# Performance work log

Measured on AMD Instinct MI355X. Metric: run time of the kernel, lower is better.

The kernel has to match this reference:

```python
import jax, jax.numpy as jnp
import numpy as np

N_MSB = 4      # bit planes
WB = 8         # weight quant bits
ABNM = 8       # activation quant bits (non-MVM)
NL = 0.1       # noise level


def quant(x, bits, r):
    # quant_pass: symmetric round-to-grid inside [-r, r]
    s = 2.0 ** (bits - 1)
    xs = jnp.clip(x / r, -1.0 + 1.0 / s, 1.0 - 1.0 / s)
    return jnp.round(xs * s) / s * r


def pact(x, a):
    # pact_a reduces to a hard clip to [-a, a]
    return jnp.clip(x, -a, a)


def bitsplit(x, n_msb):
    # x in [0,1] -> n_msb binary planes y[i] and beta weights l2/l1
    l1 = 2.0 ** n_msb - 1.0
    l2 = 2.0 ** (n_msb - 1 - jnp.arange(n_msb, dtype=x.dtype))  # [n_msb]
    y = jnp.floor(jnp.round(l1 * x)[None] / l2[:, None, None]) % 2.0  # [n_msb,B,D]
    return y, l2 / l1


def noisy_bmm(inp, W, b, key):
    # CustomMM_bmm.forward: quantized weights + additive gaussian noise
    kw, kb = jax.random.split(key)
    nw = jax.lax.stop_gradient(jax.random.normal(kw, W.shape, W.dtype) * W.max() * NL)
    nb = jax.lax.stop_gradient(jax.random.normal(kb, b.shape, b.dtype) * b.max() * NL)
    wq = quant(W, WB, 1.0)
    bq = quant(b, WB, 1.0)
    return jnp.einsum('mbi,mio->mbo', inp, wq + nw) + bq + nb  # [n_msb,B,4H]


def setup_inputs() -> dict:
    key = jax.random.key(0)
    ks = jax.random.split(key, 9)
    B, I, H, M = 4096, 256, 1024, N_MSB
    inp = {
        'input': jax.random.normal(ks[0], (B, I), jnp.float32),
        'hx': jax.random.normal(ks[1], (B, H), jnp.float32),
        'cx': jax.random.normal(ks[2], (B, H), jnp.float32),
        'weight_ih': jax.random.normal(ks[3], (M, I, 4 * H), jnp.float32),
        'weight_hh': jax.random.normal(ks[4], (M, H, 4 * H), jnp.float32),
        'bias_ih': jax.random.normal(ks[5], (M, 1, 4 * H), jnp.float32),
        'bias_hh': jax.random.normal(ks[6], (M, 1, 4 * H), jnp.float32),
        'a1': jnp.array([128.0], jnp.float32),
        'a3': jnp.array([1.0], jnp.float32),
        'a4': jnp.array([1.0], jnp.float32),
        'a5': jnp.array([1.0], jnp.float32),
        'a6': jnp.array([1.0], jnp.float32),
        'a7': jnp.array([4.0], jnp.float32),
        'a8': jnp.array([1.0], jnp.float32),
        'a9': jnp.array([4.0], jnp.float32),
        'a10': jnp.array([1.0], jnp.float32),
        'a11': jnp.array([4.0], jnp.float32),
    }
    return inp


def reference(input, hx, cx, weight_ih, weight_hh, bias_ih, bias_hh,
              a1, a3, a4, a5, a6, a7, a8, a9, a10, a11):
    k1, k2 = jax.random.split(jax.random.key(42))
    # input branch: clip -> map to [0,1] -> bit-split -> noisy bmm -> threshold -> beta-sum
    inp01 = (pact(input, a1) + a1) / (a1 * 2)
    y, beta = bitsplit(inp01, N_MSB)
    out = (noisy_bmm(y, weight_ih, bias_ih, k1) > 0.5).astype(input.dtype)
    part1 = (beta[:, None, None] * out).sum(0) * (a1 * 2) - a1
    # hidden branch (note: '+ a1' offset as in the original source)
    inp01 = (pact(hx, a11) + a1) / (a11 * 2)
    y, beta = bitsplit(inp01, N_MSB)
    out = (noisy_bmm(y, weight_hh, bias_hh, k2) > 0.5).astype(input.dtype)
    part2 = (beta[:, None, None] * out).sum(0) * (a11 * 2) - a11
    gates = part1 + part2  # [B, 4H]
    i, j, f, o = jnp.split(gates, 4, axis=1)
    fg = quant(pact(jax.nn.sigmoid(f), a3), ABNM, a3)
    ig = quant(pact(jax.nn.sigmoid(i), a4), ABNM, a4)
    act = quant(pact(jnp.tanh(j), a5), ABNM, a5)
    og = quant(pact(jax.nn.sigmoid(o), a6), ABNM, a6)
    gated_cell = quant(pact(cx * fg, a7), ABNM, a7)
    activated_input = quant(pact(ig * act, a8), ABNM, a8)
    new_c = quant(pact(gated_cell + activated_input, a9), ABNM, a9)
    activated_cell = quant(pact(jnp.tanh(new_c), a10), ABNM, a10)
    new_h = quant(pact(activated_cell * og, a11), ABNM, a11)
    return new_h, new_c
```

## Files before the change

### kernel.cpp

```cpp
#include <hip/hip_runtime.h>
#include <cstdint>
#include <cstddef>


typedef int v4i __attribute__((ext_vector_type(4)));

struct KPc { uint32_t a, b; };

__host__ __device__ constexpr KPc ctf(uint32_t k0, uint32_t k1v, uint32_t c0, uint32_t c1) {
  uint32_t ks2 = k0 ^ k1v ^ 0x1BD11BDAu;
  uint32_t x0 = c0 + k0;
  uint32_t x1 = c1 + k1v;
  uint32_t r0[4] = {13u, 15u, 26u, 6u};
  uint32_t r1[4] = {17u, 29u, 16u, 24u};
  uint32_t ks[3] = {k0, k1v, ks2};
  for (int g = 0; g < 5; ++g) {
    for (int j = 0; j < 4; ++j) {
      uint32_t rr = (g & 1) ? r1[j] : r0[j];
      x0 += x1;
      x1 = (x1 << rr) | (x1 >> (32u - rr));
      x1 ^= x0;
    }
    x0 += ks[(g + 1) % 3];
    x1 += ks[(g + 2) % 3] + (uint32_t)(g + 1);
  }
  return KPc{x0, x1};
}

constexpr KPc K1K  = ctf(0u, 42u, 0u, 0u);
constexpr KPc K2K  = ctf(0u, 42u, 0u, 1u);
constexpr KPc KWIH = ctf(K1K.a, K1K.b, 0u, 0u);
constexpr KPc KBIH = ctf(K1K.a, K1K.b, 0u, 1u);
constexpr KPc KWHH = ctf(K2K.a, K2K.b, 0u, 0u);
constexpr KPc KBHH = ctf(K2K.a, K2K.b, 0u, 1u);

__device__ __forceinline__ uint32_t tf_bits(uint32_t k0, uint32_t k1v, uint32_t j) {
  KPc r = ctf(k0, k1v, 0u, j);
  return r.a ^ r.b;
}

__device__ __forceinline__ unsigned encf(float f) {
  unsigned u = __float_as_uint(f);
  return (u & 0x80000000u) ? ~u : (u | 0x80000000u);
}
__device__ __forceinline__ float decf(unsigned e) {
  unsigned u = (e & 0x80000000u) ? (e & 0x7FFFFFFFu) : ~e;
  return __uint_as_float(u);
}

__device__ __forceinline__ void rmax_seg(const float* __restrict__ x, int n,
                                         unsigned* __restrict__ out, int rbid, int nblk) {
  unsigned best = 0u;
  for (int i = rbid * 256 + threadIdx.x; i < n; i += nblk * 256) {
    unsigned e = encf(x[i]);
    best = best > e ? best : e;
  }
  for (int off = 32; off > 0; off >>= 1) {
    unsigned o = __shfl_down(best, off, 64);
    best = best > o ? best : o;
  }
  __shared__ unsigned sm[4];
  int lane = threadIdx.x & 63, wv = threadIdx.x >> 6;
  if (lane == 0) sm[wv] = best;
  __syncthreads();
  if (threadIdx.x == 0) {
    unsigned b = sm[0];
    for (int i = 1; i < 4; ++i) b = b > sm[i] ? b : sm[i];
    atomicMax(out, b);
  }
}

__global__ void rmax_all_kernel(const float* __restrict__ wih, const float* __restrict__ whh,
                                const float* __restrict__ bih, const float* __restrict__ bhh,
                                unsigned* __restrict__ enc) {
  int b = blockIdx.x;
  if (b < 512)       rmax_seg(wih, 4 * 256 * 4096,  enc + 0, b,        512);
  else if (b < 1024) rmax_seg(whh, 4 * 1024 * 4096, enc + 1, b - 512,  512);
  else if (b < 1088) rmax_seg(bih, 16384,           enc + 2, b - 1024, 64);
  else               rmax_seg(bhh, 16384,           enc + 3, b - 1088, 64);
}

__device__ __forceinline__ float xla_log1p(float t) {
  float small = __fmul_rn(__fadd_rn(__fmul_rn(-0.5f, t), 1.0f), t);
  float large = logf(__fadd_rn(t, 1.0f));
  return (fabsf(t) < 1e-4f) ? small : large;
}

__device__ __forceinline__ float xla_erfinv(float x) {
  float w = -xla_log1p(-__fmul_rn(x, x));
  float p;
  if (w < 5.0f) {
    float ww = __fadd_rn(w, -2.5f);
    p = 2.81022636e-08f;
    p = __fadd_rn(3.43273939e-07f, __fmul_rn(p, ww));
    p = __fadd_rn(-3.5233877e-06f, __fmul_rn(p, ww));
    p = __fadd_rn(-4.39150654e-06f, __fmul_rn(p, ww));
    p = __fadd_rn(0.00021858087f, __fmul_rn(p, ww));
    p = __fadd_rn(-0.00125372503f, __fmul_rn(p, ww));
    p = __fadd_rn(-0.00417768164f, __fmul_rn(p, ww));
    p = __fadd_rn(0.246640727f, __fmul_rn(p, ww));
    p = __fadd_rn(1.50140941f, __fmul_rn(p, ww));
  } else {
    float ww = __fadd_rn(sqrtf(w), -3.0f);
    p = -0.000200214257f;
    p = __fadd_rn(0.000100950558f, __fmul_rn(p, ww));
    p = __fadd_rn(0.00134934322f, __fmul_rn(p, ww));
    p = __fadd_rn(-0.00367342844f, __fmul_rn(p, ww));
    p = __fadd_rn(0.00573950773f, __fmul_rn(p, ww));
    p = __fadd_rn(-0.0076224613f, __fmul_rn(p, ww));
    p = __fadd_rn(0.00943887047f, __fmul_rn(p, ww));
    p = __fadd_rn(1.00167406f, __fmul_rn(p, ww));
    p = __fadd_rn(2.83297682f, __fmul_rn(p, ww));
  }
  return __fmul_rn(p, x);
}

__device__ __forceinline__ float normal_from_bits(uint32_t bits) {
  float u01 = __uint_as_float((bits >> 9) | 0x3f800000u) - 1.0f;
  const float lo = -0x1.fffffep-1f;
  float u = fmaxf(lo, __fadd_rn(__fmul_rn(u01, 2.0f), lo));
  return __fmul_rn(0x1.6a09e6p+0f, xla_erfinv(u));
}

__device__ __forceinline__ float quantw(float x) {
  float xs = fminf(fmaxf(x, -0.9921875f), 0.9921875f);
  return __fmul_rn(rintf(__fmul_rn(xs, 128.0f)), 0.0078125f);
}

__device__ void do_kv(const float* __restrict__ x, const float* __restrict__ ap,
                      const float* __restrict__ offp, unsigned char* __restrict__ kvT,
                      int Kdim, int bx, int by, unsigned char* sh) {
  unsigned char (*tile)[65] = (unsigned char (*)[65])sh;
  const int tid = threadIdx.x;
  const int bt = bx * 64, it = by * 64;
  const float a = ap[0], off = offp[0];
#pragma unroll
  for (int e = 0; e < 16; ++e) {
    int idx = e * 256 + tid;
    int bl = idx >> 6, il = idx & 63;
    float v = fmaxf(-a, fminf(x[(size_t)(bt + bl) * Kdim + it + il], a));
    float t = __fdiv_rn(__fadd_rn(v, off), __fmul_rn(a, 2.0f));
    int k = (int)rintf(__fmul_rn(15.0f, t));
    tile[il][bl] = (unsigned char)(k & 15);
  }
  __syncthreads();
#pragma unroll
  for (int e = 0; e < 16; ++e) {
    int idx = e * 256 + tid;
    int il = idx >> 6, bl = idx & 63;
    kvT[(size_t)(it + il) * 4096 + bt + bl] = tile[il][bl];
  }
}

__device__ void do_aih(const float* __restrict__ input, const float* __restrict__ a1p,
                       signed char* __restrict__ A, int rbid) {
  int j = rbid * 256 + threadIdx.x;
  if (j >= 4096 * 256) return;
  float a = a1p[0];
  float v = fmaxf(-a, fminf(input[j], a));
  float t = __fdiv_rn(__fadd_rn(v, a), __fmul_rn(a, 2.0f));
  int kq = (int)rintf(__fmul_rn(15.0f, t));
  A[j]                  = (signed char)((kq >> 2) & 1);
  A[1048576 + j]        = (signed char)((kq >> 1) & 1);
  A[2097152 + j]        = (signed char)(kq & 1);
}

__device__ void do_ahh(const float* __restrict__ hx, const float* __restrict__ a11p,
                       const float* __restrict__ a1p, signed char* __restrict__ A, int rbid) {
  int j = rbid * 256 + threadIdx.x;
  if (j >= 4096 * 1024) return;
  float a = a11p[0], off = a1p[0];
  float v = fmaxf(-a, fminf(hx[j], a));
  float t = __fdiv_rn(__fadd_rn(v, off), __fmul_rn(a, 2.0f));
  int kq = (int)rintf(__fmul_rn(15.0f, t));
  A[j]                      = (signed char)((kq >> 3) & 1);
  A[(size_t)(1 << 22) + j]  = (signed char)((kq >> 2) & 1);
  A[(size_t)(2 << 22) + j]  = (signed char)((kq >> 1) & 1);
  A[(size_t)(3 << 22) + j]  = (signed char)(kq & 1);
}

__device__ void do_bias(const float* __restrict__ bsrc, float* __restrict__ bq,
                        float* __restrict__ nb, int n, const unsigned* __restrict__ encp,
                        uint32_t k0, uint32_t k1v, int rbid) {
  int j = rbid * 256 + threadIdx.x;
  if (j >= n) return;
  float bmax = decf(*encp);
  float nrm = normal_from_bits(tf_bits(k0, k1v, (uint32_t)j));
  bq[j] = quantw(bsrc[j]);
  nb[j] = __fmul_rn(__fmul_rn(nrm, bmax), 0.1f);
}

__device__ void do_t0(const float* __restrict__ W, float* __restrict__ T0,
                      const unsigned* __restrict__ encp, int rbid) {
  int j = rbid * 256 + threadIdx.x;
  if (j >= 1048576) return;
  float wmax = decf(*encp);
  float nrm = normal_from_bits(tf_bits(KWIH.a, KWIH.b, (uint32_t)j));
  float nw = __fmul_rn(__fmul_rn(nrm, wmax), 0.1f);
  T0[j] = __fadd_rn(quantw(W[j]), nw);
}

__device__ void do_bt(const float* __restrict__ W, signed char* __restrict__ Bt,
                      const unsigned* __restrict__ encp, int K, int m0, int nPlanes,
                      uint32_t k0k, uint32_t k1k, int bx, int by, int bz,
                      unsigned char* sh) {
  signed char* lhi = (signed char*)sh;
  signed char* llo = (signed char*)sh + 4352;
  const int tid = threadIdx.x;
  const int m = m0 + bz;
  const int kt = by * 64, ct = bx * 64;
  const float wmax = decf(*encp);
#pragma unroll 4
  for (int i = 0; i < 16; ++i) {
    int e = i * 256 + tid;
    int kl = e >> 6, cl = e & 63;
    uint32_t j = (uint32_t)(((m * K + kt + kl) << 12) + ct + cl);
    float nrm = normal_from_bits(tf_bits(k0k, k1k, j));
    float t = __fadd_rn(quantw(W[j]), __fmul_rn(__fmul_rn(nrm, wmax), 0.1f));
    int ti = (int)rintf(__fmul_rn(t, 6144.0f));
    int hi = (ti + 128) >> 8;
    int lo = ti - (hi << 8);
    lhi[cl * 68 + kl] = (signed char)hi;
    llo[cl * 68 + kl] = (signed char)lo;
  }
  __syncthreads();
  const size_t planeElems = (size_t)K << 12;
  signed char* bh = Bt + (size_t)bz * planeElems;
  signed char* bl = Bt + (size_t)(nPlanes + bz) * planeElems;
#pragma unroll 4
  for (int i = 0; i < 16; ++i) {
    int f = i * 256 + tid;
    int cl = f >> 6, kl = f & 63;
    size_t o = (size_t)(ct + cl) * K + kt + kl;
    bh[o] = lhi[cl * 68 + kl];
    bl[o] = llo[cl * 68 + kl];
  }
}

__global__ __launch_bounds__(256) void prep_all_kernel(
    const float* __restrict__ input, const float* __restrict__ hx,
    const float* __restrict__ wih, const float* __restrict__ whh,
    const float* __restrict__ bih, const float* __restrict__ bhh,
    const float* __restrict__ a1p, const float* __restrict__ a11p,
    const unsigned* __restrict__ enc,
    unsigned char* __restrict__ kvT, signed char* __restrict__ A_ih,
    signed char* __restrict__ A_hh, float* __restrict__ bq_ih, float* __restrict__ nb_ih,
    float* __restrict__ bq_hh, float* __restrict__ nb_hh, float* __restrict__ T0,
    signed char* __restrict__ Bt_hh, signed char* __restrict__ Bt_ih) {
  __shared__ __align__(16) unsigned char sh[8704];
  int b = blockIdx.x;
  if (b < 256) {
    do_kv(input, a1p, a1p, kvT, 256, b & 63, b >> 6, sh);
  } else if (b < 4352) {
    do_aih(input, a1p, A_ih, b - 256);
  } else if (b < 20736) {
    do_ahh(hx, a11p, a1p, A_hh, b - 4352);
  } else if (b < 20800) {
    do_bias(bih, bq_ih, nb_ih, 16384, enc + 2, KBIH.a, KBIH.b, b - 20736);
  } else if (b < 20864) {
    do_bias(bhh, bq_hh, nb_hh, 16384, enc + 3, KBHH.a, KBHH.b, b - 20800);
  } else if (b < 24960) {
    do_t0(wih, T0, enc + 0, b - 20864);
  } else if (b < 29056) {
    int t = b - 24960;
    do_bt(whh, Bt_hh, enc + 1, 1024, 0, 4, KWHH.a, KWHH.b, t & 63, (t >> 6) & 15, t >> 10, sh);
  } else {
    int t = b - 29056;
    do_bt(wih, Bt_ih, enc + 0, 256, 1, 3, KWIH.a, KWIH.b, t & 63, (t >> 6) & 3, t >> 8, sh);
  }
}

__global__ __launch_bounds__(256) void gemm_p0_kernel(
    const float* __restrict__ T0, const float* __restrict__ bq, const float* __restrict__ nb,
    const unsigned char* __restrict__ kvT, unsigned char* __restrict__ Kp) {
  const int tid = threadIdx.x, lane = tid & 63, wv = tid >> 6;
  const int c0 = blockIdx.x * 32;
  const int row = blockIdx.y * 256 + wv * 64 + lane;

  float acc[32];
#pragma unroll
  for (int j = 0; j < 32; ++j) acc[j] = 0.0f;

  const unsigned char* kvp = kvT + row;
#pragma unroll 2
  for (int k = 0; k < 256; ++k) {
    unsigned nib = kvp[(size_t)k << 12];
    float f = (float)((nib >> 3) & 1u);
    const float4* tp = (const float4*)(T0 + ((size_t)k << 12) + c0);
    float4 tv[8];
#pragma unroll
    for (int q = 0; q < 8; ++q) tv[q] = tp[q];
#pragma unroll
    for (int q = 0; q < 8; ++q) {
      acc[q * 4 + 0] = __builtin_fmaf(f, tv[q].x, acc[q * 4 + 0]);
      acc[q * 4 + 1] = __builtin_fmaf(f, tv[q].y, acc[q * 4 + 1]);
      acc[q * 4 + 2] = __builtin_fmaf(f, tv[q].z, acc[q * 4 + 2]);
      acc[q * 4 + 3] = __builtin_fmaf(f, tv[q].w, acc[q * 4 + 3]);
    }
  }

#pragma unroll
  for (int j = 0; j < 32; ++j) {
    int col = c0 + j;
    float s = __fadd_rn(__fadd_rn(acc[j], bq[col]), nb[col]);
    Kp[((size_t)row << 12) + col] = (s > 0.5f) ? (unsigned char)8 : (unsigned char)0;
  }
}

typedef __attribute__((address_space(3))) signed char lds_i8;
typedef __attribute__((address_space(1))) const signed char g_i8;

__device__ __forceinline__ void glds16(const signed char* g, signed char* l) {
  __builtin_amdgcn_global_load_lds((g_i8*)g, (lds_i8*)l, 16, 0, 0);
}

__global__ __launch_bounds__(256, 3) void gemm_mfma_kernel(
    const signed char* __restrict__ Ahh, const signed char* __restrict__ Bthh,
    const signed char* __restrict__ Aih, const signed char* __restrict__ Btih,
    const float* __restrict__ bqh, const float* __restrict__ nbh,
    const float* __restrict__ bqi, const float* __restrict__ nbi,
    unsigned char* __restrict__ Kp) {
  const int tid = threadIdx.x;
  const int lane = tid & 63, wv = tid >> 6;
  const int col0 = blockIdx.x * 64;
  const int row0 = blockIdx.y * 128;
  const int wrow = (wv >> 1) * 64;
  const int wcol = (wv & 1) * 32;

  __shared__ __align__(16) signed char smbuf[3][16384];
  const int HOFF = 8192, LOFF = 12288;

  const int l15 = lane & 15;
  const int cc  = (((lane >> 4) ^ ((lane >> 1) & 3)) << 4);
  const int xq  = ((((lane & 3) ^ ((lane >> 3) & 3))) << 4);
  const int lr  = lane >> 2;

  uint32_t k12[4][2];
#pragma unroll
  for (int rf = 0; rf < 4; ++rf) { k12[rf][0] = 0u; k12[rf][1] = 0u; }

  for (int sub = 0; sub < 7; ++sub) {
    int K, w;
    const signed char *A, *Bh, *Bl;
    const float *bqp, *nbp;
    if (sub < 4) {
      int m = sub;
      K = 1024;
      A  = Ahh  + ((size_t)m << 22);
      Bh = Bthh + ((size_t)m << 22);
      Bl = Bthh + ((size_t)(4 + m) << 22);
      bqp = bqh + (m << 12); nbp = nbh + (m << 12);
      w = (1 << (3 - m)) << 4;
    } else {
      int m = sub - 3;
      K = 256;
      A  = Aih  + ((size_t)(m - 1) << 20);
      Bh = Btih + ((size_t)(m - 1) << 20);
      Bl = Btih + ((size_t)(3 + m - 1) << 20);
      bqp = bqi + (m << 12); nbp = nbi + (m << 12);
      w = 1 << (3 - m);
    }

    const size_t soff = (size_t)lr * K + xq;
    const signed char* gA  = A  + (size_t)(row0 + 32 * wv) * K + soff;
    const signed char* gA2 = gA + (size_t)16 * K;
    const signed char* gH  = Bh + (size_t)(col0 + 16 * wv) * K + soff;
    const signed char* gL  = Bl + (size_t)(col0 + 16 * wv) * K + soff;

    auto stage = [&](signed char* base, int k0) {
      glds16(gA  + k0, base + (32 * wv) * 64);
      glds16(gA2 + k0, base + (32 * wv + 16) * 64);
      glds16(gH  + k0, base + HOFF + (16 * wv) * 64);
      glds16(gL  + k0, base + LOFF + (16 * wv) * 64);
    };

    v4i ach[4][2], acl[4][2];
    v4i zero = {0, 0, 0, 0};
#pragma unroll
    for (int rf = 0; rf < 4; ++rf)
#pragma unroll
      for (int cf = 0; cf < 2; ++cf) { ach[rf][cf] = zero; acl[rf][cf] = zero; }

    signed char* bc = &smbuf[0][0];
    signed char* bn = &smbuf[1][0];
    signed char* bf = &smbuf[2][0];

    const int nt = K >> 6;
    stage(bc, 0);
    stage(bn, 64);

    for (int t = 0; t < nt; ++t) {
      if (t + 1 < nt) {
        asm volatile("s_waitcnt vmcnt(4)" ::: "memory");
      } else {
        asm volatile("s_waitcnt vmcnt(0)" ::: "memory");
      }
      __builtin_amdgcn_s_barrier();
      __builtin_amdgcn_sched_barrier(0);
      if (t + 2 < nt) stage(bf, (t + 2) << 6);

      v4i af[4], bfh[2], bfl[2];
#pragma unroll
      for (int rf = 0; rf < 4; ++rf)
        af[rf] = *(const v4i*)(bc + (wrow + rf * 16 + l15) * 64 + cc);
#pragma unroll
      for (int cf = 0; cf < 2; ++cf) {
        bfh[cf] = *(const v4i*)(bc + HOFF + (wcol + cf * 16 + l15) * 64 + cc);
        bfl[cf] = *(const v4i*)(bc + LOFF + (wcol + cf * 16 + l15) * 64 + cc);
      }
#pragma unroll
      for (int rf = 0; rf < 4; ++rf)
#pragma unroll
        for (int cf = 0; cf < 2; ++cf) {
          ach[rf][cf] = __builtin_amdgcn_mfma_i32_16x16x64_i8(af[rf], bfh[cf], ach[rf][cf], 0, 0, 0);
          acl[rf][cf] = __builtin_amdgcn_mfma_i32_16x16x64_i8(af[rf], bfl[cf], acl[rf][cf], 0, 0, 0);
        }
      signed char* tmp = bc; bc = bn; bn = bf; bf = tmp;
    }
    __syncthreads();

#pragma unroll
    for (int cf = 0; cf < 2; ++cf) {
      int col = col0 + wcol + cf * 16 + l15;
      float bqc = bqp[col];
      float nbc = nbp[col];
#pragma unroll
      for (int rf = 0; rf < 4; ++rf)
#pragma unroll
        for (int r = 0; r < 4; ++r) {
          int tot = ach[rf][cf][r] * 256 + acl[rf][cf][r];
          float s = __fmul_rn((float)tot, (1.0f / 6144.0f));
          float s2 = __fadd_rn(__fadd_rn(s, bqc), nbc);
          if (s2 > 0.5f) k12[rf][cf] += ((uint32_t)w << (8 * r));
        }
    }
  }

#pragma unroll
  for (int rf = 0; rf < 4; ++rf)
#pragma unroll
    for (int cf = 0; cf < 2; ++cf)
#pragma unroll
      for (int r = 0; r < 4; ++r) {
        int row = row0 + wrow + rf * 16 + ((lane >> 4) << 2) + r;
        int col = col0 + wcol + cf * 16 + l15;
        size_t o = ((size_t)row << 12) + col;
        Kp[o] = (unsigned char)(Kp[o] | ((k12[rf][cf] >> (8 * r)) & 255u));
      }
}

__device__ __forceinline__ float quant8(float x, float r) {
  float xs = __fdiv_rn(x, r);
  xs = fminf(fmaxf(xs, -0.9921875f), 0.9921875f);
  float q = rintf(__fmul_rn(xs, 128.0f));
  return __fmul_rn(__fdiv_rn(q, 128.0f), r);
}
__device__ __forceinline__ float pactf(float x, float a) { return fminf(fmaxf(x, -a), a); }
__device__ __forceinline__ double sigd(double x) { return 1.0 / (1.0 + exp(-x)); }

__global__ __launch_bounds__(256) void tail_kernel(
    const unsigned char* __restrict__ Kp, const float* __restrict__ cx,
    const float* a1p, const float* a3p, const float* a4p,
    const float* a5p, const float* a6p, const float* a7p,
    const float* a8p, const float* a9p, const float* a10p,
    const float* a11p, float* __restrict__ out) {
  __shared__ float Tf[256], Ti[256], Tj[256], To[256], Tac[256];
  const int tid = threadIdx.x;
  const double a1 = (double)a1p[0], a11 = (double)a11p[0];
  const float a3 = a3p[0], a4 = a4p[0], a5 = a5p[0], a6 = a6p[0];
  const float a7 = a7p[0], a8 = a8p[0], a9 = a9p[0], a10 = a10p[0], a11f = a11p[0];

  {
    int pk = tid;
    double s1 = (double)(pk & 15) * (1.0 / 15.0);
    double s2 = (double)(pk >> 4) * (1.0 / 15.0);
    double g = (s1 * (2.0 * a1) - a1) + (s2 * (2.0 * a11) - a11);
    Tf[pk] = quant8(pactf((float)sigd(g), a3), a3);
    Ti[pk] = quant8(pactf((float)sigd(g), a4), a4);
    Tj[pk] = quant8(pactf((float)tanh(g), a5), a5);
    To[pk] = quant8(pactf((float)sigd(g), a6), a6);
    if (tid < 255) {
      float qf = (float)(tid - 127);
      float ncv = __fmul_rn(__fdiv_rn(qf, 128.0f), a9);
      Tac[tid] = quant8(pactf((float)tanh((double)ncv), a10), a10);
    }
  }
  __syncthreads();

  for (int idx = blockIdx.x * 256 + tid; idx < 4194304; idx += 2048 * 256) {
    int b = idx >> 10, h = idx & 1023;
    const unsigned char* row = Kp + (size_t)b * 4096 + h;
    int pI = row[0], pJ = row[1024], pF = row[2048], pO = row[3072];
    float fg  = Tf[pF];
    float ig  = Ti[pI];
    float act = Tj[pJ];
    float og  = To[pO];
    float cxv = cx[idx];
    float gc  = quant8(pactf(__fmul_rn(cxv, fg), a7), a7);
    float ai  = quant8(pactf(__fmul_rn(ig, act), a8), a8);
    float s   = __fadd_rn(gc, ai);
    float xs  = fminf(fmaxf(__fdiv_rn(pactf(s, a9), a9), -0.9921875f), 0.9921875f);
    float qf  = rintf(__fmul_rn(xs, 128.0f));
    float nc  = __fmul_rn(__fdiv_rn(qf, 128.0f), a9);
    float ac  = Tac[(int)qf + 127];
    float nh  = quant8(pactf(__fmul_rn(ac, og), a11f), a11f);
    out[idx] = nh;
    out[4194304 + idx] = nc;
  }
}

extern "C" void kernel_launch(void* const* d_in, const int* in_sizes, int n_in,
                              void* d_out, int out_size, void* d_ws, size_t ws_size,
                              hipStream_t stream) {
  const float* input = (const float*)d_in[0];
  const float* hx    = (const float*)d_in[1];
  const float* cx    = (const float*)d_in[2];
  const float* wih   = (const float*)d_in[3];
  const float* whh   = (const float*)d_in[4];
  const float* bih   = (const float*)d_in[5];
  const float* bhh   = (const float*)d_in[6];
  const float* a1p   = (const float*)d_in[7];
  const float* a3p   = (const float*)d_in[8];
  const float* a4p   = (const float*)d_in[9];
  const float* a5p   = (const float*)d_in[10];
  const float* a6p   = (const float*)d_in[11];
  const float* a7p   = (const float*)d_in[12];
  const float* a8p   = (const float*)d_in[13];
  const float* a9p   = (const float*)d_in[14];
  const float* a10p  = (const float*)d_in[15];
  const float* a11p  = (const float*)d_in[16];

  char* ws = (char*)d_ws;
  unsigned* enc        = (unsigned*)ws;
  float* T0            = (float*)(ws + 256);
  float* bq_ih         = (float*)(ws + 256 + 4194304);
  float* nb_ih         = bq_ih + 16384;
  float* bq_hh         = nb_ih + 16384;
  float* nb_hh         = bq_hh + 16384;
  unsigned char* kv_ih = (unsigned char*)(nb_hh + 16384);
  signed char* A_hh    = (signed char*)(kv_ih + 1048576);
  signed char* Bt_hh   = A_hh + 16777216;
  signed char* A_ih    = Bt_hh + 33554432;
  signed char* Bt_ih   = A_ih + 3145728;
  unsigned char* Kp    = (unsigned char*)(Bt_ih + 6291456);

  hipMemsetAsync(enc, 0, 64, stream);

  rmax_all_kernel<<<1152, 256, 0, stream>>>(wih, whh, bih, bhh, enc);

  prep_all_kernel<<<29824, 256, 0, stream>>>(input, hx, wih, whh, bih, bhh, a1p, a11p,
                                             enc, kv_ih, A_ih, A_hh, bq_ih, nb_ih,
                                             bq_hh, nb_hh, T0, Bt_hh, Bt_ih);

  gemm_p0_kernel<<<dim3(128, 16), 256, 0, stream>>>(T0, bq_ih, nb_ih, kv_ih, Kp);
  gemm_mfma_kernel<<<dim3(64, 32), 256, 0, stream>>>(A_hh, Bt_hh, A_ih, Bt_ih,
                                                     bq_hh, nb_hh, bq_ih, nb_ih, Kp);

  tail_kernel<<<2048, 256, 0, stream>>>(Kp, cx, a1p, a3p, a4p, a5p, a6p, a7p, a8p, a9p,
                                        a10p, a11p, (float*)d_out);
}
```

Measured before the change: 582.1 us.

## Merge plane-0 FP32 GEMM into MFMA GEMM launch and emit bitmask output

Folds the FP32 plane-0 input GEMM into the MFMA kernel's launch by interleaving its blocks (odd blocks run plane-0, even blocks run the MFMA tiles). The two can then run concurrently instead of back to back. Plane-0 results are now written as a packed 32-bit bitmask rather than per-byte Kp entries, and the tail kernel merges that bit into the gate codes. This also removes the read-modify-write of Kp in the MFMA epilogue. It adds a separate bitmask buffer and extra byte loads in the tail kernel.

```diff
diff --git a/kernel.cpp b/kernel.cpp
--- a/kernel.cpp
+++ b/kernel.cpp
@@ -270,43 +270,6 @@
   }
 }
 
-__global__ __launch_bounds__(256) void gemm_p0_kernel(
-    const float* __restrict__ T0, const float* __restrict__ bq, const float* __restrict__ nb,
-    const unsigned char* __restrict__ kvT, unsigned char* __restrict__ Kp) {
-  const int tid = threadIdx.x, lane = tid & 63, wv = tid >> 6;
-  const int c0 = blockIdx.x * 32;
-  const int row = blockIdx.y * 256 + wv * 64 + lane;
-
-  float acc[32];
-#pragma unroll
-  for (int j = 0; j < 32; ++j) acc[j] = 0.0f;
-
-  const unsigned char* kvp = kvT + row;
-#pragma unroll 2
-  for (int k = 0; k < 256; ++k) {
-    unsigned nib = kvp[(size_t)k << 12];
-    float f = (float)((nib >> 3) & 1u);
-    const float4* tp = (const float4*)(T0 + ((size_t)k << 12) + c0);
-    float4 tv[8];
-#pragma unroll
-    for (int q = 0; q < 8; ++q) tv[q] = tp[q];
-#pragma unroll
-    for (int q = 0; q < 8; ++q) {
-      acc[q * 4 + 0] = __builtin_fmaf(f, tv[q].x, acc[q * 4 + 0]);
-      acc[q * 4 + 1] = __builtin_fmaf(f, tv[q].y, acc[q * 4 + 1]);
-      acc[q * 4 + 2] = __builtin_fmaf(f, tv[q].z, acc[q * 4 + 2]);
-      acc[q * 4 + 3] = __builtin_fmaf(f, tv[q].w, acc[q * 4 + 3]);
-    }
-  }
-
-#pragma unroll
-  for (int j = 0; j < 32; ++j) {
-    int col = c0 + j;
-    float s = __fadd_rn(__fadd_rn(acc[j], bq[col]), nb[col]);
-    Kp[((size_t)row << 12) + col] = (s > 0.5f) ? (unsigned char)8 : (unsigned char)0;
-  }
-}
-
 typedef __attribute__((address_space(3))) signed char lds_i8;
 typedef __attribute__((address_space(1))) const signed char g_i8;
 
@@ -314,21 +277,62 @@
   __builtin_amdgcn_global_load_lds((g_i8*)g, (lds_i8*)l, 16, 0, 0);
 }
 
-__global__ __launch_bounds__(256, 3) void gemm_mfma_kernel(
+__global__ __launch_bounds__(256, 3) void gemm_mega_kernel(
     const signed char* __restrict__ Ahh, const signed char* __restrict__ Bthh,
     const signed char* __restrict__ Aih, const signed char* __restrict__ Btih,
     const float* __restrict__ bqh, const float* __restrict__ nbh,
     const float* __restrict__ bqi, const float* __restrict__ nbi,
-    unsigned char* __restrict__ Kp) {
+    const float* __restrict__ T0, const unsigned char* __restrict__ kvT,
+    unsigned char* __restrict__ Kp, unsigned* __restrict__ bm) {
+  __shared__ __align__(16) signed char smbuf[3][16384];
+  const int HOFF = 8192, LOFF = 12288;
+
   const int tid = threadIdx.x;
   const int lane = tid & 63, wv = tid >> 6;
-  const int col0 = blockIdx.x * 64;
-  const int row0 = blockIdx.y * 128;
+
+  if (blockIdx.x & 1) {
+    const int p = blockIdx.x >> 1;
+    const int c0 = (p & 127) * 32;
+    const int row = (p >> 7) * 256 + wv * 64 + lane;
+
+    float acc[32];
+#pragma unroll
+    for (int j = 0; j < 32; ++j) acc[j] = 0.0f;
+
+    const unsigned char* kvp = kvT + row;
+#pragma unroll 2
+    for (int k = 0; k < 256; ++k) {
+      unsigned nib = kvp[(size_t)k << 12];
+      float f = (float)((nib >> 3) & 1u);
+      const float4* tp = (const float4*)(T0 + ((size_t)k << 12) + c0);
+      float4 tv[8];
+#pragma unroll
+      for (int q = 0; q < 8; ++q) tv[q] = tp[q];
+#pragma unroll
+      for (int q = 0; q < 8; ++q) {
+        acc[q * 4 + 0] = __builtin_fmaf(f, tv[q].x, acc[q * 4 + 0]);
+        acc[q * 4 + 1] = __builtin_fmaf(f, tv[q].y, acc[q * 4 + 1]);
+        acc[q * 4 + 2] = __builtin_fmaf(f, tv[q].z, acc[q * 4 + 2]);
+        acc[q * 4 + 3] = __builtin_fmaf(f, tv[q].w, acc[q * 4 + 3]);
+      }
+    }
+
+    unsigned word = 0u;
+#pragma unroll
+    for (int j = 0; j < 32; ++j) {
+      int col = c0 + j;
+      float s = __fadd_rn(__fadd_rn(acc[j], bqi[col]), nbi[col]);
+      if (s > 0.5f) word |= (1u << j);
+    }
+    bm[(size_t)row * 128 + (c0 >> 5)] = word;
+    return;
+  }
+
+  const int mb = blockIdx.x >> 1;
+  const int col0 = (mb & 63) * 64;
+  const int row0 = (mb >> 6) * 128;
   const int wrow = (wv >> 1) * 64;
   const int wcol = (wv & 1) * 32;
-
-  __shared__ __align__(16) signed char smbuf[3][16384];
-  const int HOFF = 8192, LOFF = 12288;
 
   const int l15 = lane & 15;
   const int cc  = (((lane >> 4) ^ ((lane >> 1) & 3)) << 4);
@@ -444,8 +448,7 @@
       for (int r = 0; r < 4; ++r) {
         int row = row0 + wrow + rf * 16 + ((lane >> 4) << 2) + r;
         int col = col0 + wcol + cf * 16 + l15;
-        size_t o = ((size_t)row << 12) + col;
-        Kp[o] = (unsigned char)(Kp[o] | ((k12[rf][cf] >> (8 * r)) & 255u));
+        Kp[((size_t)row << 12) + col] = (unsigned char)((k12[rf][cf] >> (8 * r)) & 255u);
       }
 }
 
@@ -459,7 +462,8 @@
 __device__ __forceinline__ double sigd(double x) { return 1.0 / (1.0 + exp(-x)); }
 
 __global__ __launch_bounds__(256) void tail_kernel(
-    const unsigned char* __restrict__ Kp, const float* __restrict__ cx,
+    const unsigned char* __restrict__ Kp, const unsigned char* __restrict__ bmb,
+    const float* __restrict__ cx,
     const float* a1p, const float* a3p, const float* a4p,
     const float* a5p, const float* a6p, const float* a7p,
     const float* a8p, const float* a9p, const float* a10p,
@@ -490,7 +494,12 @@
   for (int idx = blockIdx.x * 256 + tid; idx < 4194304; idx += 2048 * 256) {
     int b = idx >> 10, h = idx & 1023;
     const unsigned char* row = Kp + (size_t)b * 4096 + h;
-    int pI = row[0], pJ = row[1024], pF = row[2048], pO = row[3072];
+    int base = b * 512 + (h >> 3);
+    int sh3 = h & 7;
+    int pI = row[0]    | (((bmb[base]       >> sh3) & 1) << 3);
+    int pJ = row[1024] | (((bmb[base + 128] >> sh3) & 1) << 3);
+    int pF = row[2048] | (((bmb[base + 256] >> sh3) & 1) << 3);
+    int pO = row[3072] | (((bmb[base + 384] >> sh3) & 1) << 3);
     float fg  = Tf[pF];
     float ig  = Ti[pI];
     float act = Tj[pJ];
@@ -543,6 +552,7 @@
   signed char* A_ih    = Bt_hh + 33554432;
   signed char* Bt_ih   = A_ih + 3145728;
   unsigned char* Kp    = (unsigned char*)(Bt_ih + 6291456);
+  unsigned* bm         = (unsigned*)(Kp + 16777216);
 
   hipMemsetAsync(enc, 0, 64, stream);
 
@@ -552,10 +562,11 @@
                                              enc, kv_ih, A_ih, A_hh, bq_ih, nb_ih,
                                              bq_hh, nb_hh, T0, Bt_hh, Bt_ih);
 
-  gemm_p0_kernel<<<dim3(128, 16), 256, 0, stream>>>(T0, bq_ih, nb_ih, kv_ih, Kp);
-  gemm_mfma_kernel<<<dim3(64, 32), 256, 0, stream>>>(A_hh, Bt_hh, A_ih, Bt_ih,
-                                                     bq_hh, nb_hh, bq_ih, nb_ih, Kp);
-
-  tail_kernel<<<2048, 256, 0, stream>>>(Kp, cx, a1p, a3p, a4p, a5p, a6p, a7p, a8p, a9p,
+  gemm_mega_kernel<<<4096, 256, 0, stream>>>(A_hh, Bt_hh, A_ih, Bt_ih,
+                                             bq_hh, nb_hh, bq_ih, nb_ih,
+                                             T0, kv_ih, Kp, bm);
+
+  tail_kernel<<<2048, 256, 0, stream>>>(Kp, (const unsigned char*)bm, cx,
+                                        a1p, a3p, a4p, a5p, a6p, a7p, a8p, a9p,
                                         a10p, a11p, (float*)d_out);
 }
```

After: 626.9 us. +7.7%, slower.

## Fuse LSTM tail into MFMA GEMM epilogue and bitpack plane-0 thresholds

Applied to the files above, without the earlier changes.

The int8 MFMA GEMM now tiles its columns so each block holds all four gates (i, j, f, o) for 16 hidden units. It writes its threshold bits into LDS and runs the LSTM cell tail in the same kernel, so the separate tail kernel and the 16 MB byte-wise Kp intermediate are gone. The plane-0 fp32 GEMM now stores a 1-bit-per-column bitmap instead of one byte per gate, which the fused tail reads back. This cuts global traffic and one launch, at the cost of strided B-tile loads across four gate strips and extra per-block table setup.

```diff
diff --git a/kernel.cpp b/kernel.cpp
--- a/kernel.cpp
+++ b/kernel.cpp
@@ -272,7 +272,7 @@
 
 __global__ __launch_bounds__(256) void gemm_p0_kernel(
     const float* __restrict__ T0, const float* __restrict__ bq, const float* __restrict__ nb,
-    const unsigned char* __restrict__ kvT, unsigned char* __restrict__ Kp) {
+    const unsigned char* __restrict__ kvT, unsigned* __restrict__ bm) {
   const int tid = threadIdx.x, lane = tid & 63, wv = tid >> 6;
   const int c0 = blockIdx.x * 32;
   const int row = blockIdx.y * 256 + wv * 64 + lane;
@@ -299,13 +299,24 @@
     }
   }
 
+  unsigned word = 0u;
 #pragma unroll
   for (int j = 0; j < 32; ++j) {
     int col = c0 + j;
     float s = __fadd_rn(__fadd_rn(acc[j], bq[col]), nb[col]);
-    Kp[((size_t)row << 12) + col] = (s > 0.5f) ? (unsigned char)8 : (unsigned char)0;
-  }
-}
+    if (s > 0.5f) word |= (1u << j);
+  }
+  bm[(size_t)row * 128 + (c0 >> 5)] = word;
+}
+
+__device__ __forceinline__ float quant8(float x, float r) {
+  float xs = __fdiv_rn(x, r);
+  xs = fminf(fmaxf(xs, -0.9921875f), 0.9921875f);
+  float q = rintf(__fmul_rn(xs, 128.0f));
+  return __fmul_rn(__fdiv_rn(q, 128.0f), r);
+}
+__device__ __forceinline__ float pactf(float x, float a) { return fminf(fmaxf(x, -a), a); }
+__device__ __forceinline__ double sigd(double x) { return 1.0 / (1.0 + exp(-x)); }
 
 typedef __attribute__((address_space(3))) signed char lds_i8;
 typedef __attribute__((address_space(1))) const signed char g_i8;
@@ -314,15 +325,19 @@
   __builtin_amdgcn_global_load_lds((g_i8*)g, (lds_i8*)l, 16, 0, 0);
 }
 
-__global__ __launch_bounds__(256, 3) void gemm_mfma_kernel(
+__global__ __launch_bounds__(256, 3) void gemm_mfma_tail_kernel(
     const signed char* __restrict__ Ahh, const signed char* __restrict__ Bthh,
     const signed char* __restrict__ Aih, const signed char* __restrict__ Btih,
     const float* __restrict__ bqh, const float* __restrict__ nbh,
     const float* __restrict__ bqi, const float* __restrict__ nbi,
-    unsigned char* __restrict__ Kp) {
+    const unsigned char* __restrict__ bmb, const float* __restrict__ cx,
+    const float* a1p, const float* a3p, const float* a4p,
+    const float* a5p, const float* a6p, const float* a7p,
+    const float* a8p, const float* a9p, const float* a10p,
+    const float* a11p, float* __restrict__ out) {
   const int tid = threadIdx.x;
   const int lane = tid & 63, wv = tid >> 6;
-  const int col0 = blockIdx.x * 64;
+  const int c0 = blockIdx.x * 16;
   const int row0 = blockIdx.y * 128;
   const int wrow = (wv >> 1) * 64;
   const int wcol = (wv & 1) * 32;
@@ -364,8 +379,8 @@
     const size_t soff = (size_t)lr * K + xq;
     const signed char* gA  = A  + (size_t)(row0 + 32 * wv) * K + soff;
     const signed char* gA2 = gA + (size_t)16 * K;
-    const signed char* gH  = Bh + (size_t)(col0 + 16 * wv) * K + soff;
-    const signed char* gL  = Bl + (size_t)(col0 + 16 * wv) * K + soff;
+    const signed char* gH  = Bh + (size_t)(c0 + wv * 1024) * K + soff;
+    const signed char* gL  = Bl + (size_t)(c0 + wv * 1024) * K + soff;
 
     auto stage = [&](signed char* base, int k0) {
       glds16(gA  + k0, base + (32 * wv) * 64);
@@ -421,7 +436,8 @@
 
 #pragma unroll
     for (int cf = 0; cf < 2; ++cf) {
-      int col = col0 + wcol + cf * 16 + l15;
+      int strip = (wv & 1) * 2 + cf;
+      int col = c0 + strip * 1024 + l15;
       float bqc = bqp[col];
       float nbc = nbp[col];
 #pragma unroll
@@ -436,40 +452,28 @@
     }
   }
 
+  unsigned char* gates = (unsigned char*)&smbuf[2][0];
+  float* Tf  = (float*)&smbuf[0][0];
+  float* Ti  = Tf + 256;
+  float* Tj  = Ti + 256;
+  float* To  = Tj + 256;
+  float* Tac = To + 256;
+
 #pragma unroll
   for (int rf = 0; rf < 4; ++rf)
 #pragma unroll
-    for (int cf = 0; cf < 2; ++cf)
+    for (int cf = 0; cf < 2; ++cf) {
+      int strip = (wv & 1) * 2 + cf;
 #pragma unroll
       for (int r = 0; r < 4; ++r) {
-        int row = row0 + wrow + rf * 16 + ((lane >> 4) << 2) + r;
-        int col = col0 + wcol + cf * 16 + l15;
-        size_t o = ((size_t)row << 12) + col;
-        Kp[o] = (unsigned char)(Kp[o] | ((k12[rf][cf] >> (8 * r)) & 255u));
+        int lrow = wrow + rf * 16 + ((lane >> 4) << 2) + r;
+        gates[lrow * 64 + strip * 16 + l15] = (unsigned char)((k12[rf][cf] >> (8 * r)) & 255u);
       }
-}
-
-__device__ __forceinline__ float quant8(float x, float r) {
-  float xs = __fdiv_rn(x, r);
-  xs = fminf(fmaxf(xs, -0.9921875f), 0.9921875f);
-  float q = rintf(__fmul_rn(xs, 128.0f));
-  return __fmul_rn(__fdiv_rn(q, 128.0f), r);
-}
-__device__ __forceinline__ float pactf(float x, float a) { return fminf(fmaxf(x, -a), a); }
-__device__ __forceinline__ double sigd(double x) { return 1.0 / (1.0 + exp(-x)); }
-
-__global__ __launch_bounds__(256) void tail_kernel(
-    const unsigned char* __restrict__ Kp, const float* __restrict__ cx,
-    const float* a1p, const float* a3p, const float* a4p,
-    const float* a5p, const float* a6p, const float* a7p,
-    const float* a8p, const float* a9p, const float* a10p,
-    const float* a11p, float* __restrict__ out) {
-  __shared__ float Tf[256], Ti[256], Tj[256], To[256], Tac[256];
-  const int tid = threadIdx.x;
+    }
+
   const double a1 = (double)a1p[0], a11 = (double)a11p[0];
   const float a3 = a3p[0], a4 = a4p[0], a5 = a5p[0], a6 = a6p[0];
   const float a7 = a7p[0], a8 = a8p[0], a9 = a9p[0], a10 = a10p[0], a11f = a11p[0];
-
   {
     int pk = tid;
     double s1 = (double)(pk & 15) * (1.0 / 15.0);
@@ -487,15 +491,25 @@
   }
   __syncthreads();
 
-  for (int idx = blockIdx.x * 256 + tid; idx < 4194304; idx += 2048 * 256) {
-    int b = idx >> 10, h = idx & 1023;
-    const unsigned char* row = Kp + (size_t)b * 4096 + h;
-    int pI = row[0], pJ = row[1024], pF = row[2048], pO = row[3072];
+#pragma unroll
+  for (int e = 0; e < 8; ++e) {
+    int idx = e * 256 + tid;
+    int lrow = idx >> 4;
+    int hc = idx & 15;
+    int grow = row0 + lrow;
+    int h = c0 + hc;
+    int base = grow * 512 + (h >> 3);
+    int sh3 = h & 7;
+    int pI = gates[lrow * 64 + 0  + hc] | (((bmb[base]       >> sh3) & 1) << 3);
+    int pJ = gates[lrow * 64 + 16 + hc] | (((bmb[base + 128] >> sh3) & 1) << 3);
+    int pF = gates[lrow * 64 + 32 + hc] | (((bmb[base + 256] >> sh3) & 1) << 3);
+    int pO = gates[lrow * 64 + 48 + hc] | (((bmb[base + 384] >> sh3) & 1) << 3);
     float fg  = Tf[pF];
     float ig  = Ti[pI];
     float act = Tj[pJ];
     float og  = To[pO];
-    float cxv = cx[idx];
+    int oidx = grow * 1024 + h;
+    float cxv = cx[oidx];
     float gc  = quant8(pactf(__fmul_rn(cxv, fg), a7), a7);
     float ai  = quant8(pactf(__fmul_rn(ig, act), a8), a8);
     float s   = __fadd_rn(gc, ai);
@@ -504,8 +518,8 @@
     float nc  = __fmul_rn(__fdiv_rn(qf, 128.0f), a9);
     float ac  = Tac[(int)qf + 127];
     float nh  = quant8(pactf(__fmul_rn(ac, og), a11f), a11f);
-    out[idx] = nh;
-    out[4194304 + idx] = nc;
+    out[oidx] = nh;
+    out[4194304 + oidx] = nc;
   }
 }
 
@@ -542,7 +556,7 @@
   signed char* Bt_hh   = A_hh + 16777216;
   signed char* A_ih    = Bt_hh + 33554432;
   signed char* Bt_ih   = A_ih + 3145728;
-  unsigned char* Kp    = (unsigned char*)(Bt_ih + 6291456);
+  unsigned* bm         = (unsigned*)(Bt_ih + 6291456);
 
   hipMemsetAsync(enc, 0, 64, stream);
 
@@ -552,10 +566,10 @@
                                              enc, kv_ih, A_ih, A_hh, bq_ih, nb_ih,
                                              bq_hh, nb_hh, T0, Bt_hh, Bt_ih);
 
-  gemm_p0_kernel<<<dim3(128, 16), 256, 0, stream>>>(T0, bq_ih, nb_ih, kv_ih, Kp);
-  gemm_mfma_kernel<<<dim3(64, 32), 256, 0, stream>>>(A_hh, Bt_hh, A_ih, Bt_ih,
-                                                     bq_hh, nb_hh, bq_ih, nb_ih, Kp);
-
-  tail_kernel<<<2048, 256, 0, stream>>>(Kp, cx, a1p, a3p, a4p, a5p, a6p, a7p, a8p, a9p,
-                                        a10p, a11p, (float*)d_out);
-}
+  gemm_p0_kernel<<<dim3(128, 16), 256, 0, stream>>>(T0, bq_ih, nb_ih, kv_ih, bm);
+
+  gemm_mfma_tail_kernel<<<dim3(64, 32), 256, 0, stream>>>(
+      A_hh, Bt_hh, A_ih, Bt_ih, bq_hh, nb_hh, bq_ih, nb_ih,
+      (const unsigned char*)bm, cx,
+      a1p, a3p, a4p, a5p, a6p, a7p, a8p, a9p, a10p, a11p, (float*)d_out);
+}
```

Result: no change. 589.8 us (+1.3%).
